# Kernel tuning notes

Hardware: AMD Instinct MI355X
Metric: run time of the kernel (lower is better)

## Reference

```python
import jax, jax.numpy as jnp
import numpy as np
import math

N = 50000          # nodes
E = 800000         # edges (~avg degree 16)
G = 2048           # graphs
NUM_RBF = 128
CUTOFF = 5.0       # max_radius
C_RAD = 16         # radial channels
SH_DIM = 9         # 1x0e+1x1e+1x2e
_AVG_DEGREE = 15.57930850982666
_AVG_NUM_NODES = 18.03065905448718


def spherical_harmonics_l012(vec):
    """e3nn spherical harmonics l=0,1,2, normalize=True, component normalization."""
    r = jnp.linalg.norm(vec, axis=-1, keepdims=True)
    u = vec / jnp.maximum(r, 1e-12)
    x, y, z = u[..., 0], u[..., 1], u[..., 2]
    s3, s5, s15 = math.sqrt(3.0), math.sqrt(5.0), math.sqrt(15.0)
    x2, y2, z2 = x * x, y * y, z * z
    return jnp.stack([
        jnp.ones_like(x),                 # l=0
        s3 * x, s3 * y, s3 * z,           # l=1
        s15 * x * z,                      # l=2 (e3nn ordering)
        s15 * x * y,
        s5 * (y2 - 0.5 * (x2 + z2)),
        s15 * y * z,
        (s15 / 2.0) * (z2 - x2),
    ], axis=-1)


def exp_normal_smearing(dist):
    """ExpNormalSmearing with cutoff_lower=0, cutoff_upper=CUTOFF, num_rbf=NUM_RBF."""
    alpha = 5.0 / CUTOFF
    start = math.exp(-CUTOFF)
    means = jnp.linspace(start, 1.0, NUM_RBF).astype(dist.dtype)
    beta = (2.0 / NUM_RBF * (1.0 - start)) ** (-2)
    d = dist[..., None]
    cut = 0.5 * (jnp.cos(d * math.pi / CUTOFF) + 1.0) * (d < CUTOFF).astype(d.dtype)
    return cut * jnp.exp(-beta * (jnp.exp(-alpha * d) - means) ** 2)


def setup_inputs() -> dict:
    key = jax.random.key(0)
    ks = jax.random.split(key, 16)
    s = 0.05
    return {
        "pos": jax.random.normal(ks[0], (N, 3), jnp.float32) * 2.0,
        "atom_table": jax.random.normal(ks[1], (64, C_RAD * SH_DIM), jnp.float32) * s,
        "W1": jax.random.normal(ks[2], (NUM_RBF, 64), jnp.float32) * s,
        "b1": jnp.zeros((64,), jnp.float32),
        "W2": jax.random.normal(ks[3], (64, 64), jnp.float32) * s,
        "b2": jnp.zeros((64,), jnp.float32),
        "W3": jax.random.normal(ks[4], (64, C_RAD), jnp.float32) * s,
        "Wh1": jax.random.normal(ks[5], (C_RAD * SH_DIM, C_RAD * SH_DIM), jnp.float32) * s,
        "bh1": jnp.zeros((C_RAD * SH_DIM,), jnp.float32),
        "Wh2": jax.random.normal(ks[6], (C_RAD * SH_DIM, 1), jnp.float32) * s,
        "bh2": jnp.zeros((1,), jnp.float32),
        "node_atom": jax.random.randint(ks[7], (N,), 0, 64, jnp.int32),
        "edge_src": jax.random.randint(ks[8], (E,), 0, N, jnp.int32),
        "edge_dst": jax.random.randint(ks[9], (E,), 0, N, jnp.int32),
        "batch": jnp.sort(jax.random.randint(ks[10], (N,), 0, G, jnp.int32)),
    }


def reference(pos, atom_table, W1, b1, W2, b2, W3, Wh1, bh1, Wh2, bh2,
              node_atom, edge_src, edge_dst, batch):
    # edge geometry
    edge_vec = pos[edge_src] - pos[edge_dst]                      # [E,3]
    edge_len = jnp.linalg.norm(edge_vec, axis=-1)                 # [E]
    rbf = exp_normal_smearing(edge_len)                           # [E,128]
    sh = spherical_harmonics_l012(edge_vec)                       # [E,9]

    # radial MLP (fc_neurons = [128,64,64] -> C_RAD weights)
    h = jax.nn.silu(rbf @ W1 + b1)
    h = jax.nn.silu(h @ W2 + b2)
    rad = h @ W3                                                  # [E,C_RAD]

    # RBF-conditioned tensor-product-style edge message: outer(radial, sh)
    msg = (rad[:, :, None] * sh[:, None, :]).reshape(rad.shape[0], C_RAD * SH_DIM)

    # scatter-add aggregation, rescaled by avg degree (EdgeDegreeEmbedding)
    deg_embed = jax.ops.segment_sum(msg, edge_dst, num_segments=N)
    deg_embed = deg_embed / math.sqrt(_AVG_DEGREE)                # [N,144]

    node_features = atom_table[node_atom] + deg_embed             # [N,144]

    # energy head: Linear -> SiLU -> Linear(1x0e)
    hn = jax.nn.silu(node_features @ Wh1 + bh1)
    node_energy = hn @ Wh2 + bh2                                  # [N,1]

    # ScaledScatter over graphs
    energy = jax.ops.segment_sum(node_energy, batch, num_segments=G)
    energy = energy / math.sqrt(_AVG_NUM_NODES)                   # [G,1]
    return energy
```

## Files before the change

kernel.cpp:

```cpp
#include <hip/hip_runtime.h>
#include <math.h>

#define NND 50000
#define NED 800000
#define NGR 2048
#define NT  1024
#define NB  512
#define NPB 98
#define HALF 49
#define EPB 4096
#define BIN_BLOCKS 196
#define TBL_BLOCKS 64
#define CHW 16
#define LCAP 16
#define LSTR 17
#define SCAP 2016
#define OFW 128
#define OFL 63
#define RECMASK 0x07FFFFFFu

constexpr double dSTART = 0.006737946999085467;
constexpr float  K_START = (float)dSTART;
constexpr float  K_STEP  = (float)((1.0 - dSTART) / 127.0);
constexpr float  K_BETA  = (float)(1.0 / ((2.0/128.0*(1.0-dSTART)) * (2.0/128.0*(1.0-dSTART))));
constexpr float  K_TSTEP = (float)((1.0 - dSTART) / (double)(NT - 1));
constexpr float  K_INVT  = (float)((double)(NT - 1) / (1.0 - dSTART));

__device__ __forceinline__ float silu_f(float x) {
    return x * __builtin_amdgcn_rcpf(1.0f + __expf(-x));
}

__global__ void __launch_bounds__(1024)
bin_table(const int* __restrict__ esrc, const int* __restrict__ edst,
          unsigned* __restrict__ bins, unsigned* __restrict__ ofbuf,
          const float* __restrict__ W1, const float* __restrict__ b1,
          const float* __restrict__ W2, const float* __restrict__ b2,
          const float* __restrict__ W3, float* __restrict__ table,
          float* __restrict__ out)
{
    __shared__ int      lcnt[NB];
    __shared__ unsigned lbuf[NB * LSTR];
    __shared__ int      ofcnt_l;
    __shared__ unsigned ofl[OFL * 2];
    const int bid = blockIdx.x;
    const int tid = threadIdx.x;

    if (bid < BIN_BLOCKS) {
        if (tid < NB) lcnt[tid] = 0;
        if (tid == 0) ofcnt_l = 0;
        __syncthreads();
        const int e0 = bid * EPB;
        #pragma unroll
        for (int r = 0; r < 4; ++r) {
            int e = e0 + r * 1024 + tid;
            if (e < NED) {
                int dst = edst[e];
                int src = esrc[e];
                int b = dst / NPB;
                unsigned rec = ((unsigned)src << 7) | (unsigned)(dst - b * NPB);
                int p = atomicAdd(&lcnt[b], 1);
                if (p < LCAP) lbuf[b * LSTR + p] = rec;
                else {
                    int gp = atomicAdd(&ofcnt_l, 1);
                    if (gp < OFL) { ofl[2*gp] = (unsigned)src; ofl[2*gp+1] = (unsigned)dst; }
                }
            }
        }
        __syncthreads();
        unsigned* dp = bins + (size_t)bid * NB * CHW;
        for (int i = tid; i < NB * CHW; i += 1024) {
            int b = i >> 4, k = i & 15;
            int c = lcnt[b]; c = c < LCAP ? c : LCAP;
            unsigned val;
            if (k == 0) val = ((c > 0) ? lbuf[b * LSTR] : 0u) | ((unsigned)c << 27);
            else        val = lbuf[b * LSTR + k];
            dp[i] = val;
        }
        {
            int oc = ofcnt_l; oc = oc < OFL ? oc : OFL;
            unsigned* op = ofbuf + (size_t)bid * OFW;
            if (tid == 0) op[0] = (unsigned)oc;
            for (int i = tid; i < 2 * oc; i += 1024) op[1 + i] = ofl[i];
        }
        return;
    }

    const int tb   = bid - BIN_BLOCKS;
    const int lane = tid & 63;
    const int w    = tid >> 6;
    const int ti   = tb * 16 + w;
    float* hl = (float*)lbuf + w * 68;

    if (tb < 2) out[tb * 1024 + tid] = 0.0f;

    const float xe = K_START + K_TSTEP * (float)ti;
    const float dd = -logf(xe);
    const float cutv = (dd < 5.0f) ? (0.5f * (__cosf(dd * 0.6283185307179586f) + 1.0f)) : 0.0f;

    float h1 = b1[lane];
    #pragma unroll 4
    for (int k = 0; k < 128; ++k) {
        float mean = K_START + K_STEP * (float)k;
        float t = xe - mean;
        float rk = cutv * __expf(-K_BETA * t * t);
        h1 = fmaf(rk, W1[(k << 6) + lane], h1);
    }
    hl[lane] = silu_f(h1);

    float h2 = b2[lane];
    #pragma unroll 4
    for (int k = 0; k < 64; ++k)
        h2 = fmaf(hl[k], W2[(k << 6) + lane], h2);
    float s2 = silu_f(h2);
    hl[lane] = s2;

    if (lane < 16) {
        float rad = 0.0f;
        #pragma unroll 4
        for (int k = 0; k < 64; ++k)
            rad = fmaf(hl[k], W3[(k << 4) + lane], rad);
        table[ti * 16 + lane] = rad;
    }
}

__global__ void __launch_bounds__(448)
agg_head(const float* __restrict__ pos, const unsigned* __restrict__ bins,
         const unsigned* __restrict__ ofbuf,
         const float* __restrict__ table,
         const float* __restrict__ atom_table, const int* __restrict__ node_atom,
         const int* __restrict__ batch,
         const float* __restrict__ Wh1, const float* __restrict__ bh1,
         const float* __restrict__ Wh2, const float* __restrict__ bh2,
         float* __restrict__ out, float isd, float isn)
{
    __shared__ int    lcnt[HALF], soff[HALF], scur[HALF];
    __shared__ int    ccache[BIN_BLOCKS];
    __shared__ float4 ubuf4[SCAP];
    float4* sgeo = ubuf4;
    float*  ubuf = (float*)ubuf4;
    const int tid = threadIdx.x;
    const int b   = blockIdx.x >> 1;
    const int h   = blockIdx.x & 1;
    const int lbase = h * HALF;
    const int gbase = b * NPB + lbase;

    if (tid < HALF) lcnt[tid] = 0;
    if (tid < BIN_BLOCKS)
        ccache[tid] = (int)(bins[((size_t)tid * NB + b) * CHW] >> 27);
    __syncthreads();

    const int TOT = BIN_BLOCKS * CHW;
    for (int s = tid; s < TOT; s += 448) {
        int seg = s >> 4, k = s & 15;
        if (k < ccache[seg]) {
            unsigned rec = bins[((size_t)seg * NB + b) * CHW + k] & RECMASK;
            int l = (int)(rec & 127u) - lbase;
            if (l >= 0 && l < HALF) atomicAdd(&lcnt[l], 1);
        }
    }
    for (int s = tid; s < BIN_BLOCKS * OFL; s += 448) {
        int bb = s / OFL, k = s - bb * OFL;
        int oc = (int)ofbuf[(size_t)bb * OFW];
        if (k < oc) {
            int l = (int)ofbuf[(size_t)bb * OFW + 2 + 2*k] - gbase;
            if (l >= 0 && l < HALF) atomicAdd(&lcnt[l], 1);
        }
    }
    __syncthreads();

    if (tid < 64) {
        int v = (tid < HALF) ? lcnt[tid] : 0;
        int x = v;
        #pragma unroll
        for (int off = 1; off < 64; off <<= 1) {
            int u = __shfl_up(x, off);
            if (tid >= off) x += u;
        }
        if (tid < HALF) { soff[tid] = x - v; scur[tid] = x - v; }
    }
    __syncthreads();

    for (int s = tid; s < TOT; s += 448) {
        int seg = s >> 4, k = s & 15;
        if (k >= ccache[seg]) continue;
        unsigned rec = bins[((size_t)seg * NB + b) * CHW + k] & RECMASK;
        int local = (int)(rec & 127u);
        int l = local - lbase;
        if (l < 0 || l >= HALF) continue;
        int src = (int)(rec >> 7);
        int dst = b * NPB + local;
        float vx = pos[3*src+0] - pos[3*dst+0];
        float vy = pos[3*src+1] - pos[3*dst+1];
        float vz = pos[3*src+2] - pos[3*dst+2];
        float d2 = vx*vx + vy*vy + vz*vz;
        float4 g;
        if (d2 < 25.0f) {
            float ddv = sqrtf(d2);
            float inv = 1.0f / fmaxf(ddv, 1e-12f);
            g = make_float4(vx*inv, vy*inv, vz*inv, __expf(-ddv));
        } else {
            g = make_float4(0.0f, 0.0f, 0.0f, K_START);
        }
        int p = atomicAdd(&scur[l], 1);
        if (p < SCAP) sgeo[p] = g;
    }
    for (int s = tid; s < BIN_BLOCKS * OFL; s += 448) {
        int bb = s / OFL, k = s - bb * OFL;
        int oc = (int)ofbuf[(size_t)bb * OFW];
        if (k >= oc) continue;
        int src = (int)ofbuf[(size_t)bb * OFW + 1 + 2*k];
        int dst = (int)ofbuf[(size_t)bb * OFW + 2 + 2*k];
        int l = dst - gbase;
        if (l < 0 || l >= HALF) continue;
        float vx = pos[3*src+0] - pos[3*dst+0];
        float vy = pos[3*src+1] - pos[3*dst+1];
        float vz = pos[3*src+2] - pos[3*dst+2];
        float d2 = vx*vx + vy*vy + vz*vz;
        float4 g;
        if (d2 < 25.0f) {
            float ddv = sqrtf(d2);
            float inv = 1.0f / fmaxf(ddv, 1e-12f);
            g = make_float4(vx*inv, vy*inv, vz*inv, __expf(-ddv));
        } else {
            g = make_float4(0.0f, 0.0f, 0.0f, K_START);
        }
        int p = atomicAdd(&scur[l], 1);
        if (p < SCAP) sgeo[p] = g;
    }
    __syncthreads();

    const int lane = tid & 63;
    const int w    = tid >> 6;
    const int g    = lane >> 3;
    const int c    = lane & 7;
    const int l    = w * 8 + g;
    const int gn   = gbase + l;
    const bool valid = (l < HALF) && (gn < NND);

    float acc0[9], acc1[9];
    #pragma unroll
    for (int s = 0; s < 9; ++s) { acc0[s] = 0.0f; acc1[s] = 0.0f; }

    int start = 0, end = 0;
    if (valid) {
        start = soff[l];
        end   = start + lcnt[l];
        end   = end < SCAP ? end : SCAP;
    }

    for (int p = start; p < end; ++p) {
        float4 gv = sgeo[p];
        float ux = gv.x, uy = gv.y, uz = gv.z, xe = gv.w;

        float t = (xe - K_START) * K_INVT;
        int i0 = (int)t;
        i0 = i0 < 0 ? 0 : (i0 > NT-2 ? NT-2 : i0);
        float fr = t - (float)i0;
        const float* tb = table + (size_t)i0 * 16 + c;
        float r0a = tb[0], r1a = tb[16];
        float r0b = tb[8], r1b = tb[24];
        float ra = fmaf(fr, r1a - r0a, r0a);
        float rb = fmaf(fr, r1b - r0b, r0b);

        float sh1 = 1.7320508075688772f * ux;
        float sh2 = 1.7320508075688772f * uy;
        float sh3 = 1.7320508075688772f * uz;
        float sh4 = 3.872983346207417f * ux * uz;
        float sh5 = 3.872983346207417f * ux * uy;
        float sh6 = 2.23606797749979f * (uy*uy - 0.5f*(ux*ux + uz*uz));
        float sh7 = 3.872983346207417f * uy * uz;
        float sh8 = 1.9364916731037085f * (uz*uz - ux*ux);

        acc0[0] += ra;                    acc1[0] += rb;
        acc0[1] = fmaf(ra, sh1, acc0[1]); acc1[1] = fmaf(rb, sh1, acc1[1]);
        acc0[2] = fmaf(ra, sh2, acc0[2]); acc1[2] = fmaf(rb, sh2, acc1[2]);
        acc0[3] = fmaf(ra, sh3, acc0[3]); acc1[3] = fmaf(rb, sh3, acc1[3]);
        acc0[4] = fmaf(ra, sh4, acc0[4]); acc1[4] = fmaf(rb, sh4, acc1[4]);
        acc0[5] = fmaf(ra, sh5, acc0[5]); acc1[5] = fmaf(rb, sh5, acc1[5]);
        acc0[6] = fmaf(ra, sh6, acc0[6]); acc1[6] = fmaf(rb, sh6, acc1[6]);
        acc0[7] = fmaf(ra, sh7, acc0[7]); acc1[7] = fmaf(rb, sh7, acc1[7]);
        acc0[8] = fmaf(ra, sh8, acc0[8]); acc1[8] = fmaf(rb, sh8, acc1[8]);
    }

    __syncthreads();

    float* nfw = ubuf + w * 1152;
    {
        int a = valid ? node_atom[gn] : 0;
        const float* at = atom_table + (size_t)a * 144;
        #pragma unroll
        for (int s = 0; s < 9; ++s) {
            nfw[g*144 + c*9 + s]     = fmaf(acc0[s], isd, at[c*9 + s]);
            nfw[g*144 + (c+8)*9 + s] = fmaf(acc1[s], isd, at[(c+8)*9 + s]);
        }
    }

    float A0[8], A1[8], A2[8];
    {
        float bb0 = bh1[lane], bb1 = bh1[lane + 64];
        float bb2 = (lane < 16) ? bh1[lane + 128] : 0.0f;
        #pragma unroll
        for (int q = 0; q < 8; ++q) { A0[q] = bb0; A1[q] = bb1; A2[q] = bb2; }
    }

    for (int k4 = 0; k4 < 36; ++k4) {
        float4 nq[8];
        #pragma unroll
        for (int q = 0; q < 8; ++q)
            nq[q] = *(const float4*)&nfw[q*144 + k4*4];
        const float* wrow = Wh1 + (size_t)(k4*4) * 144;
#define HSTEP(COMP, OFF) { \
        float w0 = wrow[(OFF)*144 + lane]; \
        float w1 = wrow[(OFF)*144 + lane + 64]; \
        float w2 = (lane < 16) ? wrow[(OFF)*144 + lane + 128] : 0.0f; \
        _Pragma("unroll") \
        for (int q = 0; q < 8; ++q) { \
            float nk = nq[q].COMP; \
            A0[q] = fmaf(nk, w0, A0[q]); \
            A1[q] = fmaf(nk, w1, A1[q]); \
            A2[q] = fmaf(nk, w2, A2[q]); } }
        HSTEP(x, 0) HSTEP(y, 1) HSTEP(z, 2) HSTEP(w, 3)
#undef HSTEP
    }

    float wl0 = Wh2[lane], wl1 = Wh2[lane + 64];
    float wl2 = (lane < 16) ? Wh2[lane + 128] : 0.0f;
    float bv  = bh2[0];
    #pragma unroll
    for (int q = 0; q < 8; ++q) {
        float en = silu_f(A0[q]) * wl0 + silu_f(A1[q]) * wl1;
        if (lane < 16) en = fmaf(silu_f(A2[q]), wl2, en);
        en += __shfl_down(en, 32);
        en += __shfl_down(en, 16);
        en += __shfl_down(en, 8);
        en += __shfl_down(en, 4);
        en += __shfl_down(en, 2);
        en += __shfl_down(en, 1);
        int lq = w * 8 + q;
        int gq = gbase + lq;
        if (lane == 0 && lq < HALF && gq < NND) {
            unsafeAtomicAdd(out + batch[gq], (en + bv) * isn);
        }
    }
}

extern "C" void kernel_launch(void* const* d_in, const int* in_sizes, int n_in,
                              void* d_out, int out_size, void* d_ws, size_t ws_size,
                              hipStream_t stream) {
    const float* pos        = (const float*)d_in[0];
    const float* atom_table = (const float*)d_in[1];
    const float* W1         = (const float*)d_in[2];
    const float* b1         = (const float*)d_in[3];
    const float* W2         = (const float*)d_in[4];
    const float* b2         = (const float*)d_in[5];
    const float* W3         = (const float*)d_in[6];
    const float* Wh1        = (const float*)d_in[7];
    const float* bh1        = (const float*)d_in[8];
    const float* Wh2        = (const float*)d_in[9];
    const float* bh2        = (const float*)d_in[10];
    const int*   node_atom  = (const int*)d_in[11];
    const int*   edge_src   = (const int*)d_in[12];
    const int*   edge_dst   = (const int*)d_in[13];
    const int*   batch      = (const int*)d_in[14];

    float* out = (float*)d_out;

    char*     wsb   = (char*)d_ws;
    float*    table = (float*)(wsb);
    unsigned* ofbuf = (unsigned*)(wsb + 65536);
    unsigned* bins  = (unsigned*)(wsb + 165888);

    bin_table<<<BIN_BLOCKS + TBL_BLOCKS, 1024, 0, stream>>>(
        edge_src, edge_dst, bins, ofbuf, W1, b1, W2, b2, W3, table, out);

    float isd = 1.0f / sqrtf(15.57930850982666f);
    float isn = 1.0f / sqrtf(18.03065905448718f);
    agg_head<<<NB * 2, 448, 0, stream>>>(
        pos, bins, ofbuf, table, atom_table, node_atom,
        batch, Wh1, bh1, Wh2, bh2, out, isd, isn);
}
```

Measured before the change: 221.0 us.

## Split shared geometry and node-feature buffers, drop barrier, serialize overflow scan per thread

New measurement: 194.9 us. 11.8% less time.

```diff
diff --git a/kernel.cpp b/kernel.cpp
--- a/kernel.cpp
+++ b/kernel.cpp
@@ -14,7 +14,7 @@
 #define CHW 16
 #define LCAP 16
 #define LSTR 17
-#define SCAP 2016
+#define SCAP 1152
 #define OFW 128
 #define OFL 63
 #define RECMASK 0x07FFFFFFu
@@ -135,9 +135,8 @@
 {
     __shared__ int    lcnt[HALF], soff[HALF], scur[HALF];
     __shared__ int    ccache[BIN_BLOCKS];
-    __shared__ float4 ubuf4[SCAP];
-    float4* sgeo = ubuf4;
-    float*  ubuf = (float*)ubuf4;
+    __shared__ float4 sgeo[SCAP];
+    __shared__ float  nf_s[7][8][144];
     const int tid = threadIdx.x;
     const int b   = blockIdx.x >> 1;
     const int h   = blockIdx.x & 1;
@@ -158,11 +157,11 @@
             if (l >= 0 && l < HALF) atomicAdd(&lcnt[l], 1);
         }
     }
-    for (int s = tid; s < BIN_BLOCKS * OFL; s += 448) {
-        int bb = s / OFL, k = s - bb * OFL;
-        int oc = (int)ofbuf[(size_t)bb * OFW];
-        if (k < oc) {
-            int l = (int)ofbuf[(size_t)bb * OFW + 2 + 2*k] - gbase;
+    if (tid < BIN_BLOCKS) {
+        const unsigned* op = ofbuf + (size_t)tid * OFW;
+        int oc = (int)op[0];
+        for (int k = 0; k < oc; ++k) {
+            int l = (int)op[2 + 2*k] - gbase;
             if (l >= 0 && l < HALF) atomicAdd(&lcnt[l], 1);
         }
     }
@@ -204,28 +203,29 @@
         int p = atomicAdd(&scur[l], 1);
         if (p < SCAP) sgeo[p] = g;
     }
-    for (int s = tid; s < BIN_BLOCKS * OFL; s += 448) {
-        int bb = s / OFL, k = s - bb * OFL;
-        int oc = (int)ofbuf[(size_t)bb * OFW];
-        if (k >= oc) continue;
-        int src = (int)ofbuf[(size_t)bb * OFW + 1 + 2*k];
-        int dst = (int)ofbuf[(size_t)bb * OFW + 2 + 2*k];
-        int l = dst - gbase;
-        if (l < 0 || l >= HALF) continue;
-        float vx = pos[3*src+0] - pos[3*dst+0];
-        float vy = pos[3*src+1] - pos[3*dst+1];
-        float vz = pos[3*src+2] - pos[3*dst+2];
-        float d2 = vx*vx + vy*vy + vz*vz;
-        float4 g;
-        if (d2 < 25.0f) {
-            float ddv = sqrtf(d2);
-            float inv = 1.0f / fmaxf(ddv, 1e-12f);
-            g = make_float4(vx*inv, vy*inv, vz*inv, __expf(-ddv));
-        } else {
-            g = make_float4(0.0f, 0.0f, 0.0f, K_START);
-        }
-        int p = atomicAdd(&scur[l], 1);
-        if (p < SCAP) sgeo[p] = g;
+    if (tid < BIN_BLOCKS) {
+        const unsigned* op = ofbuf + (size_t)tid * OFW;
+        int oc = (int)op[0];
+        for (int k = 0; k < oc; ++k) {
+            int src = (int)op[1 + 2*k];
+            int dst = (int)op[2 + 2*k];
+            int l = dst - gbase;
+            if (l < 0 || l >= HALF) continue;
+            float vx = pos[3*src+0] - pos[3*dst+0];
+            float vy = pos[3*src+1] - pos[3*dst+1];
+            float vz = pos[3*src+2] - pos[3*dst+2];
+            float d2 = vx*vx + vy*vy + vz*vz;
+            float4 g;
+            if (d2 < 25.0f) {
+                float ddv = sqrtf(d2);
+                float inv = 1.0f / fmaxf(ddv, 1e-12f);
+                g = make_float4(vx*inv, vy*inv, vz*inv, __expf(-ddv));
+            } else {
+                g = make_float4(0.0f, 0.0f, 0.0f, K_START);
+            }
+            int p = atomicAdd(&scur[l], 1);
+            if (p < SCAP) sgeo[p] = g;
+        }
     }
     __syncthreads();
 
@@ -282,16 +282,13 @@
         acc0[8] = fmaf(ra, sh8, acc0[8]); acc1[8] = fmaf(rb, sh8, acc1[8]);
     }
 
-    __syncthreads();
-
-    float* nfw = ubuf + w * 1152;
     {
         int a = valid ? node_atom[gn] : 0;
         const float* at = atom_table + (size_t)a * 144;
         #pragma unroll
         for (int s = 0; s < 9; ++s) {
-            nfw[g*144 + c*9 + s]     = fmaf(acc0[s], isd, at[c*9 + s]);
-            nfw[g*144 + (c+8)*9 + s] = fmaf(acc1[s], isd, at[(c+8)*9 + s]);
+            nf_s[w][g][c*9 + s]     = fmaf(acc0[s], isd, at[c*9 + s]);
+            nf_s[w][g][(c+8)*9 + s] = fmaf(acc1[s], isd, at[(c+8)*9 + s]);
         }
     }
 
@@ -307,7 +304,7 @@
         float4 nq[8];
         #pragma unroll
         for (int q = 0; q < 8; ++q)
-            nq[q] = *(const float4*)&nfw[q*144 + k4*4];
+            nq[q] = *(const float4*)&nf_s[w][q][k4*4];
         const float* wrow = Wh1 + (size_t)(k4*4) * 144;
 #define HSTEP(COMP, OFF) { \
         float w0 = wrow[(OFF)*144 + lane]; \
```
